# Optimization experiments

Hardware: AMD Instinct MI355X
Metric: run time of the kernel (lower is better)

Reference implementation:

```python
import jax, jax.numpy as jnp
import numpy as np
import math

H = 16
D_MODEL = 1024
D_K = D_MODEL // H  # 64
B = 4
S = 2048
D_V = 64


def setup_inputs() -> dict:
    key0 = jax.random.key(0)
    ks = jax.random.split(key0, 7)
    scale = 1.0 / math.sqrt(D_MODEL)
    return {
        "query": jax.random.normal(ks[0], (B, S, D_MODEL), jnp.float32),
        "key": jax.random.normal(ks[1], (B, S, D_MODEL), jnp.float32),
        "value": jax.random.normal(ks[2], (B, D_V, S), jnp.float32),
        "Wq": jax.random.normal(ks[3], (D_MODEL, D_MODEL), jnp.float32) * scale,
        "bq": jax.random.normal(ks[4], (D_MODEL,), jnp.float32) * scale,
        "Wk": jax.random.normal(ks[5], (D_MODEL, D_MODEL), jnp.float32) * scale,
        "bk": jax.random.normal(ks[6], (D_MODEL,), jnp.float32) * scale,
    }


def reference(query, key, value, Wq, bq, Wk, bk):
    nb = query.shape[0]
    # Linear projections then split heads: [B,S,d_model] -> [B,h,S,d_k]
    q = (query @ Wq.T + bq).reshape(nb, -1, H, D_K).transpose(0, 2, 1, 3)
    k = (key @ Wk.T + bk).reshape(nb, -1, H, D_K).transpose(0, 2, 1, 3)
    # value.repeat(h,1,1,1).permute(1,0,3,2): [B,dv,Sk] -> broadcast over heads
    # with last two axes swapped -> effectively v[b,s,d] = value[b,d,s]
    v = jnp.swapaxes(value, 1, 2)  # [B, Sk, dv]
    # Scaled dot-product attention (mask branch is a no-op: m == zeros)
    scores = jnp.einsum("bhqd,bhkd->bhqk", q, k) / math.sqrt(D_K)
    p_attn = jax.nn.softmax(scores, axis=-1)
    # value identical across heads, contract directly with base v
    x = jnp.einsum("bhqk,bkd->bhqd", p_attn, v)  # [B,h,Sq,dv]
    return (jnp.mean(x, axis=1), q)
```

## Files before the change

### kernel.cpp

```cpp
#include <hip/hip_runtime.h>


typedef unsigned short u16;
typedef __attribute__((ext_vector_type(8))) u16 u16x8;
typedef __attribute__((ext_vector_type(8))) __bf16 bf16x8;
typedef __attribute__((ext_vector_type(4))) float f32x4;
typedef __attribute__((ext_vector_type(16))) float f32x16;
typedef __attribute__((ext_vector_type(2))) unsigned u32x2;
typedef __attribute__((ext_vector_type(4))) unsigned u32x4;

typedef const __attribute__((address_space(1))) void gvoid;
typedef __attribute__((address_space(3))) void lvoid;

__device__ __forceinline__ void gload16(const void* g, void* l) {
  __builtin_amdgcn_global_load_lds((gvoid*)g, (lvoid*)l, 16, 0, 0);
}

__device__ __forceinline__ u16 f2bf(float f) {
  unsigned u = __builtin_bit_cast(unsigned, f);
  u += 0x7fffu + ((u >> 16) & 1u);
  return (u16)(u >> 16);
}

__device__ __forceinline__ unsigned cvtpk(float lo, float hi) {
  unsigned r;
  asm("v_cvt_pk_bf16_f32 %0, %1, %2" : "=v"(r) : "v"(lo), "v"(hi));
  return r;
}

__device__ __forceinline__ float exp2a(float x) {
  float r;
  asm("v_exp_f32 %0, %1" : "=v"(r) : "v"(x));
  return r;
}

__device__ __forceinline__ f32x16 zero16() {
  f32x16 z;
#pragma unroll
  for (int i = 0; i < 16; ++i) z[i] = 0.f;
  return z;
}

__global__ void cvt_small(const float* __restrict__ wq, const float* __restrict__ wk,
                          const float* __restrict__ v,
                          u16* __restrict__ wqb, u16* __restrict__ wkb, u16* __restrict__ vb) {
  int i = blockIdx.x * 256 + threadIdx.x;
  const float* s;
  u16* d;
  int off;
  if (i < 262144)      { s = wq; d = wqb; off = i; }
  else if (i < 524288) { s = wk; d = wkb; off = i - 262144; }
  else if (i < 655360) { s = v;  d = vb;  off = i - 524288; }
  else return;
  float4 x = reinterpret_cast<const float4*>(s)[off];
  ushort4 o;
  o.x = f2bf(x.x); o.y = f2bf(x.y); o.z = f2bf(x.z); o.w = f2bf(x.w);
  reinterpret_cast<ushort4*>(d)[off] = o;
}

__global__ __launch_bounds__(256) void proj_gemm(
    const float* __restrict__ qf, const float* __restrict__ kf,
    const u16* __restrict__ Wqb, const u16* __restrict__ Wkb,
    const float* __restrict__ bq, const float* __restrict__ bk,
    float* __restrict__ out1, u16* __restrict__ k_ws)
{
  const int z = blockIdx.z;
  const float* __restrict__ A = z ? kf : qf;
  const u16* __restrict__ W = z ? Wkb : Wqb;
  const float* __restrict__ bias = z ? bk : bq;

  __shared__ u16 As[2][128 * 64];
  __shared__ u16 Bs[2][128 * 64];

  const int tid = threadIdx.x;
  const int lane = tid & 63;
  const int w = tid >> 6;
  const int ln = lane & 15;
  const int lh = lane >> 4;
  const int wm = w >> 1, wn = w & 1;
  const int n0 = blockIdx.x * 128;
  const int j0 = blockIdx.y * 128;

  f32x4 acc[4][4];
#pragma unroll
  for (int mt = 0; mt < 4; ++mt)
#pragma unroll
    for (int nt = 0; nt < 4; ++nt)
      acc[mt][nt] = f32x4{0.f, 0.f, 0.f, 0.f};

  const int r_ = tid >> 3, c8_ = tid & 7;
  const int swz = c8_ ^ (r_ & 7);
  const int rxm = (ln & 7) << 3;

#pragma unroll
  for (int it = 0; it < 4; ++it)
    gload16(&W[(size_t)(j0 + it * 32 + r_) * 1024 + swz * 8], &Bs[0][(it * 256 + w * 64) * 8]);
#pragma unroll
  for (int j = 0; j < 4; ++j) {
    int u = tid + j * 256;
    int r = u >> 3;
    int sl = (u & 7) ^ (r & 7);
    const float* s = &A[(size_t)(n0 + r) * 1024 + (u & 7) * 8];
    float4 x0 = *reinterpret_cast<const float4*>(s);
    float4 x1 = *reinterpret_cast<const float4*>(s + 4);
    u32x4 wv{cvtpk(x0.x, x0.y), cvtpk(x0.z, x0.w), cvtpk(x1.x, x1.y), cvtpk(x1.z, x1.w)};
    *reinterpret_cast<u32x4*>(&As[0][r * 64 + sl * 8]) = wv;
  }
  __syncthreads();

  for (int kt = 0; kt < 16; ++kt) {
    const int cur = kt & 1, nb = cur ^ 1;
    float4 ax0[4], ax1[4];
    if (kt < 15) {
#pragma unroll
      for (int it = 0; it < 4; ++it)
        gload16(&W[(size_t)(j0 + it * 32 + r_) * 1024 + (kt + 1) * 64 + swz * 8],
                &Bs[nb][(it * 256 + w * 64) * 8]);
#pragma unroll
      for (int j = 0; j < 4; ++j) {
        int u = tid + j * 256;
        const float* s = &A[(size_t)(n0 + (u >> 3)) * 1024 + (kt + 1) * 64 + (u & 7) * 8];
        ax0[j] = *reinterpret_cast<const float4*>(s);
        ax1[j] = *reinterpret_cast<const float4*>(s + 4);
      }
    }
#pragma unroll
    for (int ks = 0; ks < 2; ++ks) {
      bf16x8 a[4], bfr[4];
#pragma unroll
      for (int mt = 0; mt < 4; ++mt) {
        int row = wm * 64 + mt * 16 + ln;
        a[mt] = __builtin_bit_cast(bf16x8,
            *reinterpret_cast<const u16x8*>(&As[cur][row * 64 + (((lh + ks * 4) * 8) ^ rxm)]));
      }
#pragma unroll
      for (int nt = 0; nt < 4; ++nt) {
        int row = wn * 64 + nt * 16 + ln;
        bfr[nt] = __builtin_bit_cast(bf16x8,
            *reinterpret_cast<const u16x8*>(&Bs[cur][row * 64 + (((lh + ks * 4) * 8) ^ rxm)]));
      }
      __builtin_amdgcn_s_setprio(1);
#pragma unroll
      for (int mt = 0; mt < 4; ++mt)
#pragma unroll
        for (int nt = 0; nt < 4; ++nt)
          acc[mt][nt] = __builtin_amdgcn_mfma_f32_16x16x32_bf16(a[mt], bfr[nt], acc[mt][nt], 0, 0, 0);
      __builtin_amdgcn_s_setprio(0);
    }
    if (kt < 15) {
#pragma unroll
      for (int j = 0; j < 4; ++j) {
        int u = tid + j * 256;
        int r = u >> 3;
        int sl = (u & 7) ^ (r & 7);
        u32x4 wv{cvtpk(ax0[j].x, ax0[j].y), cvtpk(ax0[j].z, ax0[j].w),
                 cvtpk(ax1[j].x, ax1[j].y), cvtpk(ax1[j].z, ax1[j].w)};
        *reinterpret_cast<u32x4*>(&As[nb][r * 64 + sl * 8]) = wv;
      }
      __syncthreads();
    }
  }

  float* Cf = (float*)&As[0][0];
  const int lane16 = tid & 15;
  const int segt = tid >> 4;
#pragma unroll
  for (int half = 0; half < 2; ++half) {
    __syncthreads();
    if (wm == half) {
#pragma unroll
      for (int nt = 0; nt < 4; ++nt) {
        int jl = wn * 64 + nt * 16 + ln;
        float bv = bias[j0 + jl];
#pragma unroll
        for (int mt = 0; mt < 4; ++mt)
#pragma unroll
          for (int r = 0; r < 4; ++r)
            Cf[(mt * 16 + lh * 4 + r) * 128 + jl] = acc[mt][nt][r] + bv;
      }
    }
    __syncthreads();
#pragma unroll
    for (int i = 0; i < 8; ++i) {
      int sidx = i * 16 + segt;
      int rowl = sidx >> 1, hh = sidx & 1;
      int n = n0 + half * 64 + rowl;
      int bidx = n >> 11, s = n & 2047;
      int hgl = (j0 + hh * 64) >> 6;
      size_t off = ((size_t)(bidx * 16 + hgl) * 2048 + s) * 64 + lane16 * 4;
      float4 v = *reinterpret_cast<const float4*>(&Cf[rowl * 128 + hh * 64 + lane16 * 4]);
      if (z == 0) {
        *reinterpret_cast<float4*>(&out1[off]) = v;
      } else {
        u32x2 pk{cvtpk(v.x, v.y), cvtpk(v.z, v.w)};
        *reinterpret_cast<u32x2*>(&k_ws[off]) = pk;
      }
    }
  }
}

#define SOFTMAX_CVT(P, PF0, PF1, LACC)                                               \
  {                                                                                  \
    _Pragma("unroll")                                                                \
    for (int r = 0; r < 16; ++r) P[r] = exp2a(P[r]);                                 \
    LACC += (((P[0]+P[1])+(P[2]+P[3])) + ((P[4]+P[5])+(P[6]+P[7])))                  \
          + (((P[8]+P[9])+(P[10]+P[11])) + ((P[12]+P[13])+(P[14]+P[15])));           \
    u32x2 sA0 = __builtin_amdgcn_permlane32_swap(cvtpk(P[0],P[1]),   cvtpk(P[4],P[5]),   false,false); \
    u32x2 sB0 = __builtin_amdgcn_permlane32_swap(cvtpk(P[2],P[3]),   cvtpk(P[6],P[7]),   false,false); \
    u32x2 sA1 = __builtin_amdgcn_permlane32_swap(cvtpk(P[8],P[9]),   cvtpk(P[12],P[13]), false,false); \
    u32x2 sB1 = __builtin_amdgcn_permlane32_swap(cvtpk(P[10],P[11]), cvtpk(P[14],P[15]), false,false); \
    u32x4 w0_{sA0[0], sB0[0], sA0[1], sB0[1]};                                       \
    u32x4 w1_{sA1[0], sB1[0], sA1[1], sB1[1]};                                       \
    PF0 = __builtin_bit_cast(bf16x8, w0_);                                           \
    PF1 = __builtin_bit_cast(bf16x8, w1_);                                           \
  }

#define ST_BLOCK(ST)                                                                 \
  {                                                                                  \
    f32x16 p = zero16();                                                             \
    __builtin_amdgcn_s_setprio(1);                                                   \
    _Pragma("unroll")                                                                \
    for (int c = 0; c < 4; ++c) {                                                    \
      int ka = bo + ((((ST * 32 + l31) * 128) + c * 32 + hi * 16) ^ xm);             \
      bf16x8 kf = __builtin_bit_cast(bf16x8, *reinterpret_cast<const u16x8*>(KtB + ka)); \
      p = __builtin_amdgcn_mfma_f32_32x32x16_bf16(kf, aq[c], p, 0, 0, 0);            \
    }                                                                                \
    __builtin_amdgcn_s_setprio(0);                                                   \
    bf16x8 pf0, pf1;                                                                 \
    SOFTMAX_CVT(p, pf0, pf1, lA);                                                    \
    _Pragma("unroll")                                                                \
    for (int kc = 0; kc < 2; ++kc) {                                                 \
      int cb = ST * 64 + kc * 32 + hi * 16;                                          \
      bf16x8 vA = __builtin_bit_cast(bf16x8,                                         \
          *reinterpret_cast<const u16x8*>(VtB + bo + ((l31 * 128 + cb) ^ xm)));      \
      bf16x8 vB = __builtin_bit_cast(bf16x8,                                         \
          *reinterpret_cast<const u16x8*>(VtB + bo + (((32 + l31) * 128 + cb) ^ xm))); \
      bf16x8 pf = kc ? pf1 : pf0;                                                    \
      __builtin_amdgcn_s_setprio(1);                                                 \
      oA = __builtin_amdgcn_mfma_f32_32x32x16_bf16(vA, pf, oA, 0, 0, 0);             \
      oB = __builtin_amdgcn_mfma_f32_32x32x16_bf16(vB, pf, oB, 0, 0, 0);             \
      __builtin_amdgcn_s_setprio(0);                                                 \
    }                                                                                \
  }

__global__ __launch_bounds__(256, 4) void attn_kernel(
    const float* __restrict__ qf, const u16* __restrict__ k_ws,
    const u16* __restrict__ valb, u16* __restrict__ x_ws)
{
  const int wgid = (blockIdx.x & 7) * 128 + (blockIdx.x >> 3);
  const int qblk = wgid & 15;
  const int h = (wgid >> 4) & 15;
  const int b = wgid >> 8;
  const int bh = b * 16 + h;

  const int tid = threadIdx.x, lane = tid & 63, w = tid >> 6;
  const int l31 = lane & 31, hi = lane >> 5;
  const int xm = (lane & 7) << 4;

  __shared__ u16 Kt[2][4096];
  __shared__ u16 Vt[2][4096];
  char* KtB = (char*)&Kt[0][0];
  char* VtB = (char*)&Vt[0][0];

  bf16x8 aq[4];
  {
    const float qs = 0.125f * 1.4426950408889634f;
    const size_t qb0 = ((size_t)bh * 2048 + qblk * 128 + w * 32 + l31) * 64;
#pragma unroll
    for (int c = 0; c < 4; ++c) {
      const float* src = &qf[qb0 + c * 16 + hi * 8];
      float4 v0 = *reinterpret_cast<const float4*>(src);
      float4 v1 = *reinterpret_cast<const float4*>(src + 4);
      u16x8 t;
      t[0] = f2bf(v0.x * qs); t[1] = f2bf(v0.y * qs);
      t[2] = f2bf(v0.z * qs); t[3] = f2bf(v0.w * qs);
      t[4] = f2bf(v1.x * qs); t[5] = f2bf(v1.y * qs);
      t[6] = f2bf(v1.z * qs); t[7] = f2bf(v1.w * qs);
      aq[c] = __builtin_bit_cast(bf16x8, t);
    }
  }

  const u16* kg = k_ws + (size_t)bh * 131072;
  const u16* vg = valb + (size_t)b * 131072;
  const int u0 = tid, u1 = tid + 256;
  const u16* ks0 = kg + (u0 >> 3) * 64 + ((u0 ^ (u0 >> 3)) & 7) * 8;
  const u16* ks1 = kg + (u1 >> 3) * 64 + ((u1 ^ (u1 >> 3)) & 7) * 8;
  const u16* vs0 = vg + (u0 >> 3) * 2048 + ((u0 ^ (u0 >> 3)) & 7) * 8;
  const u16* vs1 = vg + (u1 >> 3) * 2048 + ((u1 ^ (u1 >> 3)) & 7) * 8;
  u16* kd0 = &Kt[0][(w * 64) * 8];
  u16* kd1 = &Kt[0][(256 + w * 64) * 8];
  u16* vd0 = &Vt[0][(w * 64) * 8];
  u16* vd1 = &Vt[0][(256 + w * 64) * 8];

  gload16(ks0, kd0); gload16(ks1, kd1);
  gload16(vs0, vd0); gload16(vs1, vd1);

  float lA = 0.0f;
  f32x16 oA = zero16(), oB = zero16();
  int cur = 0;
  __syncthreads();

  for (int t = 0; t < 32; ++t) {
    if (t < 31) {
      int nb = (cur ^ 1) * 4096;
      size_t ko = (size_t)(t + 1) * 4096;
      int vo = (t + 1) * 64;
      gload16(ks0 + ko, kd0 + nb); gload16(ks1 + ko, kd1 + nb);
      gload16(vs0 + vo, vd0 + nb); gload16(vs1 + vo, vd1 + nb);
    }
    const int bo = cur * 8192;

    ST_BLOCK(0)
    ST_BLOCK(1)

    __syncthreads();
    cur ^= 1;
  }

  float lr = lA + __shfl_xor(lA, 32);
  float inv = 1.0f / lr;
  size_t ob0 = ((size_t)bh * 2048 + qblk * 128 + w * 32 + l31) * 64;
#pragma unroll
  for (int g = 0; g < 4; ++g) {
    u32x2 aa{cvtpk(oA[g*4+0]*inv, oA[g*4+1]*inv), cvtpk(oA[g*4+2]*inv, oA[g*4+3]*inv)};
    u32x2 bb{cvtpk(oB[g*4+0]*inv, oB[g*4+1]*inv), cvtpk(oB[g*4+2]*inv, oB[g*4+3]*inv)};
    *reinterpret_cast<u32x2*>(&x_ws[ob0 + g * 8 + hi * 4]) = aa;
    *reinterpret_cast<u32x2*>(&x_ws[ob0 + 32 + g * 8 + hi * 4]) = bb;
  }
}

__global__ void mean_heads(const u16* __restrict__ x_ws, float* __restrict__ out0) {
  int i = blockIdx.x * 256 + threadIdx.x;
  int d0 = (i & 7) * 8;
  int s = (i >> 3) & 2047;
  int b = i >> 14;
  float acc[8];
#pragma unroll
  for (int j = 0; j < 8; ++j) acc[j] = 0.f;
#pragma unroll
  for (int h = 0; h < 16; ++h) {
    u16x8 v = *reinterpret_cast<const u16x8*>(
        &x_ws[(((size_t)(b * 16 + h) * 2048 + s) << 6) + d0]);
#pragma unroll
    for (int j = 0; j < 8; ++j)
      acc[j] += __builtin_bit_cast(float, (unsigned)v[j] << 16);
  }
  float4 o0{acc[0] * 0.0625f, acc[1] * 0.0625f, acc[2] * 0.0625f, acc[3] * 0.0625f};
  float4 o1{acc[4] * 0.0625f, acc[5] * 0.0625f, acc[6] * 0.0625f, acc[7] * 0.0625f};
  size_t ob = ((size_t)(b * 2048 + s) << 6) + d0;
  *reinterpret_cast<float4*>(&out0[ob]) = o0;
  *reinterpret_cast<float4*>(&out0[ob + 4]) = o1;
}

extern "C" void kernel_launch(void* const* d_in, const int* in_sizes, int n_in,
                              void* d_out, int out_size, void* d_ws, size_t ws_size,
                              hipStream_t stream) {
  (void)in_sizes; (void)n_in; (void)out_size; (void)ws_size;
  const float* query = (const float*)d_in[0];
  const float* key   = (const float*)d_in[1];
  const float* value = (const float*)d_in[2];
  const float* Wq    = (const float*)d_in[3];
  const float* bq    = (const float*)d_in[4];
  const float* Wk    = (const float*)d_in[5];
  const float* bk    = (const float*)d_in[6];

  float* out0 = (float*)d_out;
  float* out1 = out0 + 524288;

  char* ws = (char*)d_ws;
  const size_t MB = 1u << 20;
  u16* x_ws = (u16*)(ws + 0);
  u16* Wqb  = (u16*)(ws + 32 * MB);
  u16* Wkb  = (u16*)(ws + 34 * MB);
  u16* valb = (u16*)(ws + 36 * MB);
  u16* k_ws = (u16*)(ws + 37 * MB);

  cvt_small<<<2560, 256, 0, stream>>>(Wq, Wk, value, Wqb, Wkb, valb);
  proj_gemm<<<dim3(64, 8, 2), 256, 0, stream>>>(query, key, Wqb, Wkb, bq, bk, out1, k_ws);
  attn_kernel<<<1024, 256, 0, stream>>>(out1, k_ws, valb, x_ws);
  mean_heads<<<256, 256, 0, stream>>>(x_ws, out0);
}
```

Before: 148.2 us.

## Load K and V fragments directly from global memory, drop LDS staging

Removes the double-buffered LDS staging of K and V tiles, which used async global-to-LDS loads and a block barrier each iteration. Each lane now reads its MFMA operand fragments straight from global memory, and the occupancy hint in launch bounds is dropped. This removes the barriers and LDS traffic. In exchange, K/V data is no longer shared through LDS across the four waves, so global and L2 traffic rises, and load latency sits on each wave's critical path with no explicit prefetch.

```diff
diff --git a/kernel.cpp b/kernel.cpp
--- a/kernel.cpp
+++ b/kernel.cpp
@@ -215,35 +215,36 @@
     PF1 = __builtin_bit_cast(bf16x8, w1_);                                           \
   }
 
-#define ST_BLOCK(ST)                                                                 \
+#define ST_BLOCK(T, ST)                                                              \
   {                                                                                  \
+    const u16* krow = kg + (size_t)((T) * 64 + (ST) * 32 + l31) * 64 + hi * 8;       \
+    bf16x8 kf0 = __builtin_bit_cast(bf16x8, *reinterpret_cast<const u16x8*>(krow));  \
+    bf16x8 kf1 = __builtin_bit_cast(bf16x8, *reinterpret_cast<const u16x8*>(krow + 16)); \
+    bf16x8 kf2 = __builtin_bit_cast(bf16x8, *reinterpret_cast<const u16x8*>(krow + 32)); \
+    bf16x8 kf3 = __builtin_bit_cast(bf16x8, *reinterpret_cast<const u16x8*>(krow + 48)); \
     f32x16 p = zero16();                                                             \
     __builtin_amdgcn_s_setprio(1);                                                   \
-    _Pragma("unroll")                                                                \
-    for (int c = 0; c < 4; ++c) {                                                    \
-      int ka = bo + ((((ST * 32 + l31) * 128) + c * 32 + hi * 16) ^ xm);             \
-      bf16x8 kf = __builtin_bit_cast(bf16x8, *reinterpret_cast<const u16x8*>(KtB + ka)); \
-      p = __builtin_amdgcn_mfma_f32_32x32x16_bf16(kf, aq[c], p, 0, 0, 0);            \
-    }                                                                                \
+    p = __builtin_amdgcn_mfma_f32_32x32x16_bf16(kf0, aq[0], p, 0, 0, 0);             \
+    p = __builtin_amdgcn_mfma_f32_32x32x16_bf16(kf1, aq[1], p, 0, 0, 0);             \
+    p = __builtin_amdgcn_mfma_f32_32x32x16_bf16(kf2, aq[2], p, 0, 0, 0);             \
+    p = __builtin_amdgcn_mfma_f32_32x32x16_bf16(kf3, aq[3], p, 0, 0, 0);             \
     __builtin_amdgcn_s_setprio(0);                                                   \
+    const u16* vrow = vg + (size_t)l31 * 2048 + (T) * 64 + (ST) * 32 + hi * 8;       \
+    bf16x8 vA0 = __builtin_bit_cast(bf16x8, *reinterpret_cast<const u16x8*>(vrow));  \
+    bf16x8 vB0 = __builtin_bit_cast(bf16x8, *reinterpret_cast<const u16x8*>(vrow + 65536)); \
+    bf16x8 vA1 = __builtin_bit_cast(bf16x8, *reinterpret_cast<const u16x8*>(vrow + 16)); \
+    bf16x8 vB1 = __builtin_bit_cast(bf16x8, *reinterpret_cast<const u16x8*>(vrow + 16 + 65536)); \
     bf16x8 pf0, pf1;                                                                 \
     SOFTMAX_CVT(p, pf0, pf1, lA);                                                    \
-    _Pragma("unroll")                                                                \
-    for (int kc = 0; kc < 2; ++kc) {                                                 \
-      int cb = ST * 64 + kc * 32 + hi * 16;                                          \
-      bf16x8 vA = __builtin_bit_cast(bf16x8,                                         \
-          *reinterpret_cast<const u16x8*>(VtB + bo + ((l31 * 128 + cb) ^ xm)));      \
-      bf16x8 vB = __builtin_bit_cast(bf16x8,                                         \
-          *reinterpret_cast<const u16x8*>(VtB + bo + (((32 + l31) * 128 + cb) ^ xm))); \
-      bf16x8 pf = kc ? pf1 : pf0;                                                    \
-      __builtin_amdgcn_s_setprio(1);                                                 \
-      oA = __builtin_amdgcn_mfma_f32_32x32x16_bf16(vA, pf, oA, 0, 0, 0);             \
-      oB = __builtin_amdgcn_mfma_f32_32x32x16_bf16(vB, pf, oB, 0, 0, 0);             \
-      __builtin_amdgcn_s_setprio(0);                                                 \
-    }                                                                                \
-  }
-
-__global__ __launch_bounds__(256, 4) void attn_kernel(
+    __builtin_amdgcn_s_setprio(1);                                                   \
+    oA = __builtin_amdgcn_mfma_f32_32x32x16_bf16(vA0, pf0, oA, 0, 0, 0);             \
+    oB = __builtin_amdgcn_mfma_f32_32x32x16_bf16(vB0, pf0, oB, 0, 0, 0);             \
+    oA = __builtin_amdgcn_mfma_f32_32x32x16_bf16(vA1, pf1, oA, 0, 0, 0);             \
+    oB = __builtin_amdgcn_mfma_f32_32x32x16_bf16(vB1, pf1, oB, 0, 0, 0);             \
+    __builtin_amdgcn_s_setprio(0);                                                   \
+  }
+
+__global__ __launch_bounds__(256) void attn_kernel(
     const float* __restrict__ qf, const u16* __restrict__ k_ws,
     const u16* __restrict__ valb, u16* __restrict__ x_ws)
 {
@@ -255,12 +256,6 @@
 
   const int tid = threadIdx.x, lane = tid & 63, w = tid >> 6;
   const int l31 = lane & 31, hi = lane >> 5;
-  const int xm = (lane & 7) << 4;
-
-  __shared__ u16 Kt[2][4096];
-  __shared__ u16 Vt[2][4096];
-  char* KtB = (char*)&Kt[0][0];
-  char* VtB = (char*)&Vt[0][0];
 
   bf16x8 aq[4];
   {
@@ -282,39 +277,13 @@
 
   const u16* kg = k_ws + (size_t)bh * 131072;
   const u16* vg = valb + (size_t)b * 131072;
-  const int u0 = tid, u1 = tid + 256;
-  const u16* ks0 = kg + (u0 >> 3) * 64 + ((u0 ^ (u0 >> 3)) & 7) * 8;
-  const u16* ks1 = kg + (u1 >> 3) * 64 + ((u1 ^ (u1 >> 3)) & 7) * 8;
-  const u16* vs0 = vg + (u0 >> 3) * 2048 + ((u0 ^ (u0 >> 3)) & 7) * 8;
-  const u16* vs1 = vg + (u1 >> 3) * 2048 + ((u1 ^ (u1 >> 3)) & 7) * 8;
-  u16* kd0 = &Kt[0][(w * 64) * 8];
-  u16* kd1 = &Kt[0][(256 + w * 64) * 8];
-  u16* vd0 = &Vt[0][(w * 64) * 8];
-  u16* vd1 = &Vt[0][(256 + w * 64) * 8];
-
-  gload16(ks0, kd0); gload16(ks1, kd1);
-  gload16(vs0, vd0); gload16(vs1, vd1);
 
   float lA = 0.0f;
   f32x16 oA = zero16(), oB = zero16();
-  int cur = 0;
-  __syncthreads();
 
   for (int t = 0; t < 32; ++t) {
-    if (t < 31) {
-      int nb = (cur ^ 1) * 4096;
-      size_t ko = (size_t)(t + 1) * 4096;
-      int vo = (t + 1) * 64;
-      gload16(ks0 + ko, kd0 + nb); gload16(ks1 + ko, kd1 + nb);
-      gload16(vs0 + vo, vd0 + nb); gload16(vs1 + vo, vd1 + nb);
-    }
-    const int bo = cur * 8192;
-
-    ST_BLOCK(0)
-    ST_BLOCK(1)
-
-    __syncthreads();
-    cur ^= 1;
+    ST_BLOCK(t, 0)
+    ST_BLOCK(t, 1)
   }
 
   float lr = lA + __shfl_xor(lA, 32);
```

Result: slower. 306.8 us (+107.1%).
